# Optimization experiments

Measured on AMD Instinct MI355X. Metric: run time of the kernel, lower is better.

The kernel has to match this reference:

```python
import jax, jax.numpy as jnp
import numpy as np

E = 2          # e_layers
DM = 64        # d_model == emb_dim (hardcoded 64 in out_layer)
H = 8          # n_heads
DH = DM // H
DFF = 256      # d_ff
P = 16         # patch_size
STRIDE = P // 2
SL = 4096      # seq_len
NPATCH = (SL - P) // STRIDE + 1   # 511
PRED = 96
B, M = 8, 8
FACTOR = 5
EPS = 1e-5


def setup_inputs() -> dict:
    key = jax.random.key(0)
    ks = jax.random.split(key, 32)
    s = jnp.float32(0.02)
    f = lambda i, shape: jax.random.normal(ks[i], shape, jnp.float32)
    d = {
        "x_enc": f(0, (B, SL, M)),
        "x_mark_enc": f(1, (B, SL, 4)),
        "x_dec": f(2, (B, PRED, M)),
        "x_mark_dec": f(3, (B, PRED, 4)),
        # patch embedding  Linear(patch_size -> emb_dim)
        "in_W": f(4, (DM, P)) * s,
        "in_b": jnp.zeros((DM,), jnp.float32),
        # per-layer attention projections (stacked over e_layers)
        "Wq": f(5, (E, DM, DM)) * s, "bq": jnp.zeros((E, DM), jnp.float32),
        "Wk": f(6, (E, DM, DM)) * s, "bk": jnp.zeros((E, DM), jnp.float32),
        "Wv": f(7, (E, DM, DM)) * s, "bv": jnp.zeros((E, DM), jnp.float32),
        "Wo": f(8, (E, DM, DM)) * s, "bo": jnp.zeros((E, DM), jnp.float32),
        # FFN (Conv1d kernel=1 == Linear)
        "c1_W": f(9, (E, DFF, DM)) * s, "c1_b": jnp.zeros((E, DFF), jnp.float32),
        "c2_W": f(10, (E, DM, DFF)) * s, "c2_b": jnp.zeros((E, DM), jnp.float32),
        # layer norms
        "ln1_g": jnp.ones((E, DM), jnp.float32), "ln1_b": jnp.zeros((E, DM), jnp.float32),
        "ln2_g": jnp.ones((E, DM), jnp.float32), "ln2_b": jnp.zeros((E, DM), jnp.float32),
        "lnf_g": jnp.ones((DM,), jnp.float32), "lnf_b": jnp.zeros((DM,), jnp.float32),
        # decode head  Linear(64*num_patches -> pred_len)
        "out_W": f(11, (PRED, DM * NPATCH)) * s,
        "out_b": jnp.zeros((PRED,), jnp.float32),
    }
    return d


def _ln(x, g, b):
    mu = x.mean(-1, keepdims=True)
    var = ((x - mu) ** 2).mean(-1, keepdims=True)
    return (x - mu) * jax.lax.rsqrt(var + EPS) * g + b


def _prob_attn(q, k, v, key):
    # q,k,v: [Bn, H, L, Dh]  (ProbSparse attention, mask_flag=False)
    Bn, h, Lq, Dh = q.shape
    Lk = k.shape[2]
    U_part = min(int(FACTOR * np.ceil(np.log(Lk))), Lk)   # sampled keys per query
    u = min(int(FACTOR * np.ceil(np.log(Lq))), Lq)        # top-u active queries
    idx = jax.random.randint(key, (Lq, U_part), 0, Lk)
    k_sample = k[:, :, idx, :]                             # [Bn,H,Lq,U,Dh]
    qk_sample = jnp.einsum('bhld,bhlud->bhlu', q, k_sample)
    # sparsity measure: max - sum/L_K (as in torch code)
    sparsity = qk_sample.max(-1) - qk_sample.sum(-1) / jnp.float32(Lk)
    _, top_idx = jax.lax.top_k(sparsity, u)                # [Bn,H,u]
    q_red = jnp.take_along_axis(q, top_idx[..., None], axis=2)  # [Bn,H,u,Dh]
    scale = jax.lax.rsqrt(jnp.float32(Dh))
    scores = jnp.einsum('bhud,bhkd->bhuk', q_red, k) * scale    # [Bn,H,u,Lk]
    attn = jax.nn.softmax(scores, axis=-1)
    # lazy context: mean of V for inactive queries, attn@V for active ones
    ctx = jnp.broadcast_to(v.mean(axis=2, keepdims=True), q.shape)
    upd = jnp.einsum('bhuk,bhkd->bhud', attn, v)
    bi = jnp.arange(Bn)[:, None, None]
    hi = jnp.arange(h)[None, :, None]
    ctx = ctx.at[bi, hi, top_idx].set(upd)
    return ctx.transpose(0, 2, 1, 3)  # [Bn,L,H,Dh]


def reference(x_enc, x_mark_enc, x_dec, x_mark_dec, in_W, in_b, Wq, bq, Wk, bk,
              Wv, bv, Wo, bo, c1_W, c1_b, c2_W, c2_b, ln1_g, ln1_b, ln2_g, ln2_b,
              lnf_g, lnf_b, out_W, out_b):
    Bb, L, Mm = x_enc.shape
    x = x_enc.transpose(0, 2, 1)  # b l m -> b m l
    pidx = jnp.arange(NPATCH)[:, None] * STRIDE + jnp.arange(P)[None, :]
    patches = x[:, :, pidx]                         # [B,M,N,P] (unfold)
    z = patches.reshape(Bb * Mm, NPATCH, P) @ in_W.T + in_b  # [BM,N,DM]
    akey = jax.random.key(1)
    for e in range(E):
        q = (z @ Wq[e].T + bq[e]).reshape(Bb * Mm, NPATCH, H, DH).transpose(0, 2, 1, 3)
        k = (z @ Wk[e].T + bk[e]).reshape(Bb * Mm, NPATCH, H, DH).transpose(0, 2, 1, 3)
        v = (z @ Wv[e].T + bv[e]).reshape(Bb * Mm, NPATCH, H, DH).transpose(0, 2, 1, 3)
        ctx = _prob_attn(q, k, v, jax.random.fold_in(akey, e))
        new_x = ctx.reshape(Bb * Mm, NPATCH, DM) @ Wo[e].T + bo[e]
        x1 = _ln(z + new_x, ln1_g[e], ln1_b[e])
        y = jax.nn.gelu(x1 @ c1_W[e].T + c1_b[e], approximate=False)
        y = y @ c2_W[e].T + c2_b[e]
        z = _ln(x1 + y, ln2_g[e], ln2_b[e])
    z = _ln(z, lnf_g, lnf_b)
    out = z.reshape(Bb * Mm, -1) @ out_W.T + out_b   # [BM, pred_len]
    out = out.reshape(Bb, Mm, PRED).transpose(0, 2, 1)  # (b m) l -> b l m
    return out[:, -PRED:, :]
```

## Files before the change

### kernel.cpp

```cpp
#include <hip/hip_runtime.h>
#include <hip/hip_bf16.h>
#include <stdint.h>
#include <math.h>

typedef __hip_bfloat16 bf16;
typedef __attribute__((ext_vector_type(8))) short short8;
typedef __attribute__((ext_vector_type(4))) short short4v;
typedef __attribute__((ext_vector_type(4))) float fx4;

#define NP 511
#define UPART 35
#define NTOK 32704
#define NBITS 17885
#define LN_EPS 1e-5f

__host__ __device__ __forceinline__ void tf2x32(uint32_t k0, uint32_t k1,
                                                uint32_t x0, uint32_t x1,
                                                uint32_t* o0, uint32_t* o1) {
  uint32_t ks2 = k0 ^ k1 ^ 0x1BD11BDAu;
  x0 += k0; x1 += k1;
#define TFR(r) { x0 += x1; x1 = (x1 << (r)) | (x1 >> (32 - (r))); x1 ^= x0; }
  TFR(13) TFR(15) TFR(26) TFR(6)   x0 += k1;  x1 += ks2 + 1u;
  TFR(17) TFR(29) TFR(16) TFR(24)  x0 += ks2; x1 += k0 + 2u;
  TFR(13) TFR(15) TFR(26) TFR(6)   x0 += k0;  x1 += k1 + 3u;
  TFR(17) TFR(29) TFR(16) TFR(24)  x0 += k1;  x1 += ks2 + 4u;
  TFR(13) TFR(15) TFR(26) TFR(6)   x0 += ks2; x1 += k0 + 5u;
#undef TFR
  *o0 = x0; *o1 = x1;
}

__device__ __forceinline__ float ldin(const void* p, int i, int f32) {
  if (f32) return ((const float*)p)[i];
  return __bfloat162float(((const bf16*)p)[i]);
}
__device__ __forceinline__ unsigned short f2bf(float v) {
  uint32_t u = __builtin_bit_cast(uint32_t, v);
  u += 0x7fffu + ((u >> 16) & 1u);
  return (unsigned short)(u >> 16);
}
__device__ __forceinline__ float bfb2f(uint32_t h) {
  uint32_t u = h << 16;
  return __builtin_bit_cast(float, u);
}
__device__ __forceinline__ float lo16(uint32_t w) { return bfb2f(w & 0xFFFFu); }
__device__ __forceinline__ float hi16(uint32_t w) { return bfb2f(w >> 16); }
__device__ __forceinline__ uint32_t pack2(float a, float b) {
  return (uint32_t)f2bf(a) | ((uint32_t)f2bf(b) << 16);
}
__device__ __forceinline__ int lanes_below(unsigned long long m) {
  return __builtin_amdgcn_mbcnt_hi((uint32_t)(m >> 32),
         __builtin_amdgcn_mbcnt_lo((uint32_t)m, 0));
}

__global__ void zero_out_kernel(bf16* __restrict__ out, int n) {
  int i = blockIdx.x * 256 + threadIdx.x;
  if (i < n) out[i] = __float2bfloat16(0.f);
}

__global__ void gen_idx_kernel(int* __restrict__ idxT,
    uint32_t ka0, uint32_t ka1, uint32_t kb0, uint32_t kb1,
    const uint32_t* __restrict__ lnfg, int* __restrict__ flag) {
  if (blockIdx.x == 0 && threadIdx.x == 0)
    flag[0] = (lnfg[0] == 0x3F800000u) ? 1 : 0;
  int i = blockIdx.x * 256 + threadIdx.x;
  if (i >= 2 * NBITS) return;
  int e = i / NBITS;
  uint32_t j = (uint32_t)(i - e * NBITS);
  uint32_t k0 = e ? kb0 : ka0, k1 = e ? kb1 : ka1;
  uint32_t o0, o1;
  tf2x32(k0, k1, 0u, j, &o0, &o1);
  uint32_t bits = o1;
  uint32_t hi = bits >> 16, lo = bits & 0xFFFFu;
  uint32_t off = ((hi % 511u) * 32u + (lo % 511u)) % 511u;
  int l = (int)(j / UPART), u = (int)(j % UPART);
  idxT[e * NBITS + u * NP + l] = (int)off;
}

__global__ __launch_bounds__(256) void embed_kernel(
    const void* __restrict__ xe, const void* __restrict__ inW,
    const void* __restrict__ inb, float* __restrict__ z,
    const int* __restrict__ flg) {
  __shared__ float xs[136 * 8];
  int f = flg[0];
  int b = blockIdx.x >> 5, nt = blockIdx.x & 31;
  int n0 = nt * 16;
  for (int i = threadIdx.x; i < 1088; i += 256) {
    int row = i >> 3, m = i & 7;
    int g = n0 * 8 + row;
    xs[i] = (g < 4096) ? ldin(xe, (b * 4096 + g) * 8 + m, f) : 0.f;
  }
  int d = threadIdx.x & 63, mg = threadIdx.x >> 6;
  float wreg[16];
#pragma unroll
  for (int p = 0; p < 16; ++p) wreg[p] = ldin(inW, d * 16 + p, f);
  float bd = ldin(inb, d, f);
  __syncthreads();
  for (int nl = 0; nl < 16; ++nl) {
    int n = n0 + nl;
    if (n >= NP) break;
#pragma unroll
    for (int mm = 0; mm < 2; ++mm) {
      int m = mg * 2 + mm;
      float acc = bd;
#pragma unroll
      for (int p = 0; p < 16; ++p)
        acc = fmaf(xs[(nl * 8 + p) * 8 + m], wreg[p], acc);
      int t = (b * 8 + m) * NP + n;
      z[(size_t)t * 64 + d] = acc;
    }
  }
}

__global__ __launch_bounds__(256) void qkv_kernel(
    const float* __restrict__ z,
    const void* __restrict__ Wq, const void* __restrict__ bq,
    const void* __restrict__ Wk, const void* __restrict__ bk,
    const void* __restrict__ Wv, const void* __restrict__ bv,
    bf16* __restrict__ qb, bf16* __restrict__ kb, bf16* __restrict__ vb,
    const int* __restrict__ flg, int e) {
  __shared__ short xb[64 * 72];
  __shared__ short wL[192 * 72];
  __shared__ float bqs[192];
  int f = flg[0];
  int t0 = blockIdx.x * 64;
  int tid = threadIdx.x;
  {
    const float4* xg = (const float4*)(z + (size_t)t0 * 64);
#pragma unroll
    for (int r = 0; r < 4; ++r) {
      int i4 = r * 256 + tid;
      float4 v = xg[i4];
      int t = (i4 * 4) >> 6, d = (i4 * 4) & 63;
      short4v h;
      h.x = (short)f2bf(v.x); h.y = (short)f2bf(v.y);
      h.z = (short)f2bf(v.z); h.w = (short)f2bf(v.w);
      *(short4v*)&xb[t * 72 + d] = h;
    }
  }
  if (!f) {
    const uint4* Wg0 = (const uint4*)((const bf16*)Wq + e * 4096);
    const uint4* Wg1 = (const uint4*)((const bf16*)Wk + e * 4096);
    const uint4* Wg2 = (const uint4*)((const bf16*)Wv + e * 4096);
#pragma unroll
    for (int r = 0; r < 2; ++r) {
      int i = r * 256 + tid;
      int row = i >> 3, c8 = (i & 7) * 8;
      *(uint4*)&wL[row * 72 + c8] = Wg0[i];
      *(uint4*)&wL[(64 + row) * 72 + c8] = Wg1[i];
      *(uint4*)&wL[(128 + row) * 72 + c8] = Wg2[i];
    }
  } else {
#pragma unroll
    for (int r = 0; r < 16; ++r) {
      int i = r * 256 + tid;
      int row = i >> 6, c = i & 63;
      wL[row * 72 + c] = (short)f2bf(((const float*)Wq)[e * 4096 + i]);
      wL[(64 + row) * 72 + c] = (short)f2bf(((const float*)Wk)[e * 4096 + i]);
      wL[(128 + row) * 72 + c] = (short)f2bf(((const float*)Wv)[e * 4096 + i]);
    }
  }
  if (tid < 192) {
    int t3 = tid >> 6, j = tid & 63;
    bqs[tid] = (t3 == 0) ? ldin(bq, e * 64 + j, f)
             : (t3 == 1) ? ldin(bk, e * 64 + j, f)
                         : ldin(bv, e * 64 + j, f);
  }
  __syncthreads();
  int lane = tid & 63, w = tid >> 6;
  int m0 = w * 16, col = lane & 15, quad = lane >> 4;
  short8 a0 = *(const short8*)&xb[(m0 + col) * 72 + quad * 8];
  short8 a1 = *(const short8*)&xb[(m0 + col) * 72 + 32 + quad * 8];
#pragma unroll
  for (int nt = 0; nt < 12; ++nt) {
    fx4 acc = {0.f, 0.f, 0.f, 0.f};
    short8 b0 = *(const short8*)&wL[(nt * 16 + col) * 72 + quad * 8];
    short8 b1 = *(const short8*)&wL[(nt * 16 + col) * 72 + 32 + quad * 8];
    acc = __builtin_amdgcn_mfma_f32_16x16x32_bf16(a0, b0, acc, 0, 0, 0);
    acc = __builtin_amdgcn_mfma_f32_16x16x32_bf16(a1, b1, acc, 0, 0, 0);
    int c = nt * 16 + col;
    int t3 = c >> 6, hd = c & 63, h = hd >> 3, d2 = hd & 7;
    bf16* base = (t3 == 0) ? qb : (t3 == 1) ? kb : vb;
    float bia = bqs[c];
#pragma unroll
    for (int reg = 0; reg < 4; ++reg) {
      int tok = t0 + m0 + quad * 4 + reg;
      int bm = tok / NP, n = tok - bm * NP;
      base[((size_t)(bm * 8 + h) * NP + n) * 8 + d2] =
          __float2bfloat16(acc[reg] + bia);
    }
  }
}

__global__ __launch_bounds__(1024, 8) void attn_fused_kernel(
    const bf16* __restrict__ qg, const bf16* __restrict__ kg,
    const bf16* __restrict__ vg, const int* __restrict__ idxT,
    bf16* __restrict__ ctx) {
  __shared__ uint32_t kkp[NP * 5 + 5];
  __shared__ uint32_t kvp[NP * 5 + 5];
  __shared__ float spars[512];
  __shared__ float mxB_s[512], smB_s[512];
  __shared__ float redv[256];
  __shared__ int topi[UPART];
  __shared__ float vmean[8];
  __shared__ unsigned char selflag[NP + 1];
  int bh = blockIdx.x;
  int bm = bh >> 3, h = bh & 7;
  size_t hb = (size_t)bh * NP * 8;
  int tid = threadIdx.x;
  int lane = tid & 63, wv = tid >> 6;
  if (tid < 512) {
    if (tid < NP) {
      uint4 b = ((const uint4*)(kg + hb))[tid];
      uint32_t* dk = kkp + tid * 5;
      dk[0] = b.x; dk[1] = b.y; dk[2] = b.z; dk[3] = b.w;
    }
  } else {
    int n = tid - 512;
    if (n < NP) {
      uint4 c = ((const uint4*)(vg + hb))[n];
      uint32_t* dv = kvp + n * 5;
      dv[0] = c.x; dv[1] = c.y; dv[2] = c.z; dv[3] = c.w;
    }
  }
  __syncthreads();
  float mxA = -1e30f, smA = 0.f;
  if (tid < NP) {
    int l = tid;
    uint4 a = ((const uint4*)(qg + hb))[l];
    float ql[8];
    ql[0] = lo16(a.x); ql[1] = hi16(a.x);
    ql[2] = lo16(a.y); ql[3] = hi16(a.y);
    ql[4] = lo16(a.z); ql[5] = hi16(a.z);
    ql[6] = lo16(a.w); ql[7] = hi16(a.w);
#pragma unroll 6
    for (int u = 0; u < 18; ++u) {
      int j = idxT[u * NP + l];
      j = ((unsigned)j > 510u) ? 0 : j;
      const uint32_t* kr = kkp + j * 5;
      uint32_t w0 = kr[0], w1 = kr[1], w2 = kr[2], w3 = kr[3];
      float dt = 0.f;
      dt = fmaf(ql[0], lo16(w0), dt); dt = fmaf(ql[1], hi16(w0), dt);
      dt = fmaf(ql[2], lo16(w1), dt); dt = fmaf(ql[3], hi16(w1), dt);
      dt = fmaf(ql[4], lo16(w2), dt); dt = fmaf(ql[5], hi16(w2), dt);
      dt = fmaf(ql[6], lo16(w3), dt); dt = fmaf(ql[7], hi16(w3), dt);
      mxA = fmaxf(mxA, dt); smA += dt;
    }
  } else if (tid >= 512 && tid < 512 + NP) {
    int l = tid - 512;
    uint4 a = ((const uint4*)(qg + hb))[l];
    float ql[8];
    ql[0] = lo16(a.x); ql[1] = hi16(a.x);
    ql[2] = lo16(a.y); ql[3] = hi16(a.y);
    ql[4] = lo16(a.z); ql[5] = hi16(a.z);
    ql[6] = lo16(a.w); ql[7] = hi16(a.w);
    float mxB = -1e30f, smB = 0.f;
#pragma unroll 6
    for (int u = 18; u < 35; ++u) {
      int j = idxT[u * NP + l];
      j = ((unsigned)j > 510u) ? 0 : j;
      const uint32_t* kr = kkp + j * 5;
      uint32_t w0 = kr[0], w1 = kr[1], w2 = kr[2], w3 = kr[3];
      float dt = 0.f;
      dt = fmaf(ql[0], lo16(w0), dt); dt = fmaf(ql[1], hi16(w0), dt);
      dt = fmaf(ql[2], lo16(w1), dt); dt = fmaf(ql[3], hi16(w1), dt);
      dt = fmaf(ql[4], lo16(w2), dt); dt = fmaf(ql[5], hi16(w2), dt);
      dt = fmaf(ql[6], lo16(w3), dt); dt = fmaf(ql[7], hi16(w3), dt);
      mxB = fmaxf(mxB, dt); smB += dt;
    }
    mxB_s[l] = mxB; smB_s[l] = smB;
  }
  __syncthreads();
  if (tid < NP) {
    spars[tid] = fmaxf(mxA, mxB_s[tid]) - (smA + smB_s[tid]) * (1.0f / 511.0f);
  } else if (tid >= 512 && tid < 768) {
    int tt = tid - 512;
    int d = tt & 7, pt = tt >> 3;
    int c = d >> 1, odd = d & 1;
    float s = 0.f;
    for (int n = pt; n < NP; n += 32) {
      uint32_t w = kvp[n * 5 + c];
      s += odd ? hi16(w) : lo16(w);
    }
    redv[tt] = s;
  }
  __syncthreads();
  if (tid < 64) {
    uint32_t key[8];
#pragma unroll
    for (int jj = 0; jj < 8; ++jj) {
      int ll = lane + jj * 64;
      if (ll < NP) {
        uint32_t u = __builtin_bit_cast(uint32_t, spars[ll]);
        key[jj] = (u & 0x80000000u) ? ~u : (u | 0x80000000u);
      } else key[jj] = 0u;
    }
    uint32_t p = 0u;
    for (int b = 31; b >= 0; --b) {
      uint32_t t = p | (1u << b);
      int cnt = 0;
#pragma unroll
      for (int jj = 0; jj < 8; ++jj)
        cnt += __popcll(__ballot(key[jj] >= t));
      if (cnt >= UPART) p = t;
    }
    int c1 = 0;
#pragma unroll
    for (int jj = 0; jj < 8; ++jj)
      c1 += __popcll(__ballot(key[jj] > p));
    int need = UPART - c1;
    int base = 0, taken = 0;
#pragma unroll
    for (int jj = 0; jj < 8; ++jj) {
      int ll = lane + jj * 64;
      bool gt = key[jj] > p;
      bool eq = key[jj] == p;
      unsigned long long meq = __ballot(eq);
      int beq = lanes_below(meq);
      bool sel = gt || (eq && (taken + beq) < need);
      unsigned long long msel = __ballot(sel);
      int pos = base + lanes_below(msel);
      if (sel) topi[pos] = ll;
      if (ll < NP) selflag[ll] = sel ? 1 : 0;
      base += __popcll(msel);
      taken += __popcll(meq);
    }
  } else if (tid >= 64 && tid < 72) {
    int d = tid - 64;
    float s = 0.f;
#pragma unroll
    for (int pt = 0; pt < 32; ++pt) s += redv[pt * 8 + d];
    vmean[d] = s * (1.0f / 511.0f);
  }
  __syncthreads();
  size_t cb = (size_t)bm * (NP * 64) + h * 8;
  if (tid < NP && !selflag[tid]) {
    uint4 pv;
    pv.x = pack2(vmean[0], vmean[1]);
    pv.y = pack2(vmean[2], vmean[3]);
    pv.z = pack2(vmean[4], vmean[5]);
    pv.w = pack2(vmean[6], vmean[7]);
    *(uint4*)(ctx + cb + (size_t)tid * 64) = pv;
  }
  const float scale = 0.35355339059327373f;
  int l0 = topi[wv];
  int l1 = topi[wv + 16];
  bool has3 = (wv + 32) < UPART;
  int l2 = has3 ? topi[wv + 32] : l0;
  l0 = ((unsigned)l0 > 510u) ? 0 : l0;
  l1 = ((unsigned)l1 > 510u) ? 0 : l1;
  l2 = ((unsigned)l2 > 510u) ? 0 : l2;
  const uint4* q4p = (const uint4*)(qg + hb);
  uint4 qv0 = q4p[l0];
  uint4 qv1 = q4p[l1];
  uint4 qv2 = q4p[l2];

  auto process = [&](uint4 a, int lsel) {
    float qs[8];
    qs[0] = lo16(a.x); qs[1] = hi16(a.x);
    qs[2] = lo16(a.y); qs[3] = hi16(a.y);
    qs[4] = lo16(a.z); qs[5] = hi16(a.z);
    qs[6] = lo16(a.w); qs[7] = hi16(a.w);
    float sreg[8];
    float mx = -1e30f;
#pragma unroll
    for (int s = 0; s < 8; ++s) {
      int j = lane + s * 64;
      int jc = (j > 510) ? 0 : j;
      const uint32_t* kr = kkp + jc * 5;
      uint32_t w0 = kr[0], w1 = kr[1], w2 = kr[2], w3 = kr[3];
      float d0 = qs[0] * lo16(w0);
      d0 = fmaf(qs[1], hi16(w0), d0);
      d0 = fmaf(qs[2], lo16(w1), d0);
      d0 = fmaf(qs[3], hi16(w1), d0);
      float d1 = qs[4] * lo16(w2);
      d1 = fmaf(qs[5], hi16(w2), d1);
      d1 = fmaf(qs[6], lo16(w3), d1);
      d1 = fmaf(qs[7], hi16(w3), d1);
      float sc = (d0 + d1) * scale;
      sreg[s] = (j > 510) ? -1e30f : sc;
      mx = fmaxf(mx, sreg[s]);
    }
    for (int off = 32; off; off >>= 1) mx = fmaxf(mx, __shfl_xor(mx, off));
    float ssum = 0.f, acc[8];
#pragma unroll
    for (int d2 = 0; d2 < 8; ++d2) acc[d2] = 0.f;
#pragma unroll
    for (int s = 0; s < 8; ++s) {
      int j = lane + s * 64;
      int jc = (j > 510) ? 0 : j;
      float w = __expf(sreg[s] - mx);
      ssum += w;
      const uint32_t* vr = kvp + jc * 5;
      uint32_t x0 = vr[0], x1 = vr[1], x2 = vr[2], x3 = vr[3];
      acc[0] = fmaf(w, lo16(x0), acc[0]); acc[1] = fmaf(w, hi16(x0), acc[1]);
      acc[2] = fmaf(w, lo16(x1), acc[2]); acc[3] = fmaf(w, hi16(x1), acc[3]);
      acc[4] = fmaf(w, lo16(x2), acc[4]); acc[5] = fmaf(w, hi16(x2), acc[5]);
      acc[6] = fmaf(w, lo16(x3), acc[6]); acc[7] = fmaf(w, hi16(x3), acc[7]);
    }
    for (int off = 32; off; off >>= 1) {
      ssum += __shfl_xor(ssum, off);
#pragma unroll
      for (int d2 = 0; d2 < 8; ++d2) acc[d2] += __shfl_xor(acc[d2], off);
    }
    if (lane == 0) {
      float inv = 1.0f / ssum;
      uint4 pv;
      pv.x = pack2(acc[0] * inv, acc[1] * inv);
      pv.y = pack2(acc[2] * inv, acc[3] * inv);
      pv.z = pack2(acc[4] * inv, acc[5] * inv);
      pv.w = pack2(acc[6] * inv, acc[7] * inv);
      *(uint4*)(ctx + cb + (size_t)lsel * 64) = pv;
    }
  };
  process(qv0, l0);
  process(qv1, l1);
  if (has3) process(qv2, l2);
}

__global__ __launch_bounds__(256) void oproj_ln_kernel(
    const float* __restrict__ z, const bf16* __restrict__ ctx,
    const void* __restrict__ Wo, const void* __restrict__ bo,
    const void* __restrict__ g, const void* __restrict__ bb,
    float* __restrict__ x1, const int* __restrict__ flg, int e) {
  __shared__ short cbL[64 * 72];
  __shared__ short woL[64 * 72];
  __shared__ float zf[64 * 64];
  __shared__ float bos[64], gs[64], bbs[64];
  int f = flg[0];
  int t0 = blockIdx.x * 64;
  int tid = threadIdx.x;
  {
    const uint4* cg = (const uint4*)(ctx + (size_t)t0 * 64);
#pragma unroll
    for (int r = 0; r < 2; ++r) {
      int i = r * 256 + tid;
      uint4 v = cg[i];
      int row = i >> 3, c8 = (i & 7) * 8;
      *(uint4*)&cbL[row * 72 + c8] = v;
    }
    const float4* zg = (const float4*)(z + (size_t)t0 * 64);
#pragma unroll
    for (int r = 0; r < 4; ++r) {
      int i4 = r * 256 + tid;
      float4 v = zg[i4];
      int t = (i4 * 4) >> 6, d = (i4 * 4) & 63;
      *(float4*)&zf[t * 64 + d] = v;
    }
  }
  if (!f) {
    const uint4* Wg = (const uint4*)((const bf16*)Wo + e * 4096);
#pragma unroll
    for (int r = 0; r < 2; ++r) {
      int i = r * 256 + tid;
      int row = i >> 3, c8 = (i & 7) * 8;
      *(uint4*)&woL[row * 72 + c8] = Wg[i];
    }
  } else {
#pragma unroll
    for (int r = 0; r < 16; ++r) {
      int i = r * 256 + tid;
      int row = i >> 6, c = i & 63;
      woL[row * 72 + c] = (short)f2bf(((const float*)Wo)[e * 4096 + i]);
    }
  }
  if (tid < 64) {
    bos[tid] = ldin(bo, e * 64 + tid, f);
    gs[tid] = ldin(g, e * 64 + tid, f);
    bbs[tid] = ldin(bb, e * 64 + tid, f);
  }
  __syncthreads();
  int lane = tid & 63, w = tid >> 6;
  int m0 = w * 16, col = lane & 15, quad = lane >> 4;
  short8 a0 = *(const short8*)&cbL[(m0 + col) * 72 + quad * 8];
  short8 a1 = *(const short8*)&cbL[(m0 + col) * 72 + 32 + quad * 8];
  fx4 vacc[4];
#pragma unroll
  for (int nt = 0; nt < 4; ++nt) {
    fx4 acc = {0.f, 0.f, 0.f, 0.f};
    short8 b0 = *(const short8*)&woL[(nt * 16 + col) * 72 + quad * 8];
    short8 b1 = *(const short8*)&woL[(nt * 16 + col) * 72 + 32 + quad * 8];
    acc = __builtin_amdgcn_mfma_f32_16x16x32_bf16(a0, b0, acc, 0, 0, 0);
    acc = __builtin_amdgcn_mfma_f32_16x16x32_bf16(a1, b1, acc, 0, 0, 0);
    vacc[nt] = acc;
  }
  float vals[4][4];
  float ps[4], sq[4];
#pragma unroll
  for (int reg = 0; reg < 4; ++reg) { ps[reg] = 0.f; sq[reg] = 0.f; }
#pragma unroll
  for (int nt = 0; nt < 4; ++nt) {
    int d = nt * 16 + col;
#pragma unroll
    for (int reg = 0; reg < 4; ++reg) {
      int tl = m0 + quad * 4 + reg;
      float v = vacc[nt][reg] + bos[d] + zf[tl * 64 + d];
      vals[nt][reg] = v;
      ps[reg] += v; sq[reg] += v * v;
    }
  }
#pragma unroll
  for (int off = 1; off < 16; off <<= 1) {
#pragma unroll
    for (int reg = 0; reg < 4; ++reg) {
      ps[reg] += __shfl_xor(ps[reg], off);
      sq[reg] += __shfl_xor(sq[reg], off);
    }
  }
#pragma unroll
  for (int reg = 0; reg < 4; ++reg) {
    float mu = ps[reg] * (1.0f / 64.0f);
    float var = sq[reg] * (1.0f / 64.0f) - mu * mu;
    float rs = rsqrtf(fmaxf(var, 0.f) + LN_EPS);
    int tl = m0 + quad * 4 + reg;
#pragma unroll
    for (int nt = 0; nt < 4; ++nt) {
      int d = nt * 16 + col;
      x1[(size_t)(t0 + tl) * 64 + d] = (vals[nt][reg] - mu) * rs * gs[d] + bbs[d];
    }
  }
}

__global__ __launch_bounds__(256) void ffn_kernel(
    const float* __restrict__ x1,
    const void* __restrict__ W1, const void* __restrict__ b1,
    const void* __restrict__ W2, const void* __restrict__ b2,
    const void* __restrict__ g, const void* __restrict__ bb,
    float* __restrict__ zo, bf16* __restrict__ zfT,
    const void* __restrict__ lfg, const void* __restrict__ lfb,
    const int* __restrict__ flg, int e, int last) {
  __shared__ __align__(16) char smem[72960];
  short* wA  = (short*)smem;
  short* rB  = (short*)(smem + 36864);
  float* b1s = (float*)(smem + 70656);
  float* b2s = b1s + 256;
  float* gs  = b2s + 64;
  float* bbs = gs + 64;
  float* g2s = bbs + 64;
  float* bb2s = g2s + 64;
  int f = flg[0];
  int t0 = blockIdx.x * 64;
  int tid = threadIdx.x;
  {
    const float4* xg = (const float4*)(x1 + (size_t)t0 * 64);
#pragma unroll
    for (int r = 0; r < 4; ++r) {
      int i4 = r * 256 + tid;
      float4 v = xg[i4];
      int t = (i4 * 4) >> 6, d = (i4 * 4) & 63;
      short4v h;
      h.x = (short)f2bf(v.x); h.y = (short)f2bf(v.y);
      h.z = (short)f2bf(v.z); h.w = (short)f2bf(v.w);
      *(short4v*)&rB[t * 72 + d] = h;
    }
  }
  if (!f) {
    const uint4* W1g = (const uint4*)((const bf16*)W1 + e * 16384);
#pragma unroll
    for (int r = 0; r < 8; ++r) {
      int i = r * 256 + tid;
      uint4 v = W1g[i];
      int j = i >> 3, k = (i & 7) * 8;
      *(uint4*)&wA[j * 72 + k] = v;
    }
  } else {
    for (int r = 0; r < 64; ++r) {
      int i = r * 256 + tid;
      int j = i >> 6, k = i & 63;
      wA[j * 72 + k] = (short)f2bf(((const float*)W1)[e * 16384 + i]);
    }
  }
  b1s[tid] = ldin(b1, e * 256 + tid, f);
  if (tid < 64) {
    b2s[tid] = ldin(b2, e * 64 + tid, f);
    gs[tid] = ldin(g, e * 64 + tid, f);
    bbs[tid] = ldin(bb, e * 64 + tid, f);
    g2s[tid] = ldin(lfg, tid, f);
    bb2s[tid] = ldin(lfb, tid, f);
  }
  __syncthreads();

  int lane = tid & 63, w = tid >> 6;
  int m0 = w * 16;
  int col = lane & 15, quad = lane >> 4;
  short8 a0 = *(const short8*)&rB[(m0 + col) * 72 + quad * 8];
  short8 a1 = *(const short8*)&rB[(m0 + col) * 72 + 32 + quad * 8];
  __syncthreads();
#pragma unroll 4
  for (int nt = 0; nt < 16; ++nt) {
    fx4 acc = {0.f, 0.f, 0.f, 0.f};
    short8 bf0 = *(const short8*)&wA[(nt * 16 + col) * 72 + quad * 8];
    short8 bf1 = *(const short8*)&wA[(nt * 16 + col) * 72 + 32 + quad * 8];
    acc = __builtin_amdgcn_mfma_f32_16x16x32_bf16(a0, bf0, acc, 0, 0, 0);
    acc = __builtin_amdgcn_mfma_f32_16x16x32_bf16(a1, bf1, acc, 0, 0, 0);
    int j = nt * 16 + col;
    float bj = b1s[j];
#pragma unroll
    for (int reg = 0; reg < 4; ++reg) {
      float a = acc[reg] + bj;
      float ge = 0.5f * a * (1.0f + erff(a * 0.70710678118654752f));
      rB[(m0 + quad * 4 + reg) * 264 + j] = (short)f2bf(ge);
    }
  }
  __syncthreads();
  if (!f) {
    const uint4* W2g = (const uint4*)((const bf16*)W2 + e * 16384);
#pragma unroll
    for (int r = 0; r < 8; ++r) {
      int i = r * 256 + tid;
      uint4 v2 = W2g[i];
      int dd = i >> 5, c = (i & 31) * 8;
      *(uint4*)&wA[dd * 264 + c] = v2;
    }
  } else {
    for (int r = 0; r < 64; ++r) {
      int i = r * 256 + tid;
      int dd = i >> 8, c = i & 255;
      wA[dd * 264 + c] = (short)f2bf(((const float*)W2)[e * 16384 + i]);
    }
  }
  __syncthreads();
  short8 af[8];
#pragma unroll
  for (int kt = 0; kt < 8; ++kt)
    af[kt] = *(const short8*)&rB[(m0 + col) * 264 + kt * 32 + quad * 8];
  fx4 vacc[4];
#pragma unroll
  for (int nt = 0; nt < 4; ++nt) {
    fx4 acc = {0.f, 0.f, 0.f, 0.f};
#pragma unroll
    for (int kt = 0; kt < 8; ++kt) {
      short8 bfr = *(const short8*)&wA[(nt * 16 + col) * 264 + kt * 32 + quad * 8];
      acc = __builtin_amdgcn_mfma_f32_16x16x32_bf16(af[kt], bfr, acc, 0, 0, 0);
    }
    vacc[nt] = acc;
  }
  float vals[4][4];
  float ps[4], sq[4];
#pragma unroll
  for (int reg = 0; reg < 4; ++reg) { ps[reg] = 0.f; sq[reg] = 0.f; }
#pragma unroll
  for (int nt = 0; nt < 4; ++nt) {
    int d = nt * 16 + col;
#pragma unroll
    for (int reg = 0; reg < 4; ++reg) {
      int tl = m0 + quad * 4 + reg;
      float v = vacc[nt][reg] + b2s[d] + x1[(size_t)(t0 + tl) * 64 + d];
      vals[nt][reg] = v;
      ps[reg] += v; sq[reg] += v * v;
    }
  }
#pragma unroll
  for (int off = 1; off < 16; off <<= 1) {
#pragma unroll
    for (int reg = 0; reg < 4; ++reg) {
      ps[reg] += __shfl_xor(ps[reg], off);
      sq[reg] += __shfl_xor(sq[reg], off);
    }
  }
  if (!last) {
#pragma unroll
    for (int reg = 0; reg < 4; ++reg) {
      float mu = ps[reg] * (1.0f / 64.0f);
      float var = sq[reg] * (1.0f / 64.0f) - mu * mu;
      float rs = rsqrtf(fmaxf(var, 0.f) + LN_EPS);
      int tl = m0 + quad * 4 + reg;
#pragma unroll
      for (int nt = 0; nt < 4; ++nt) {
        int d = nt * 16 + col;
        zo[(size_t)(t0 + tl) * 64 + d] = (vals[nt][reg] - mu) * rs * gs[d] + bbs[d];
      }
    }
  } else {
    float ps2[4], sq2[4];
#pragma unroll
    for (int reg = 0; reg < 4; ++reg) { ps2[reg] = 0.f; sq2[reg] = 0.f; }
    float v2s[4][4];
#pragma unroll
    for (int reg = 0; reg < 4; ++reg) {
      float mu = ps[reg] * (1.0f / 64.0f);
      float var = sq[reg] * (1.0f / 64.0f) - mu * mu;
      float rs = rsqrtf(fmaxf(var, 0.f) + LN_EPS);
#pragma unroll
      for (int nt = 0; nt < 4; ++nt) {
        int d = nt * 16 + col;
        float v2 = (vals[nt][reg] - mu) * rs * gs[d] + bbs[d];
        v2s[nt][reg] = v2;
        ps2[reg] += v2; sq2[reg] += v2 * v2;
      }
    }
#pragma unroll
    for (int off = 1; off < 16; off <<= 1) {
#pragma unroll
      for (int reg = 0; reg < 4; ++reg) {
        ps2[reg] += __shfl_xor(ps2[reg], off);
        sq2[reg] += __shfl_xor(sq2[reg], off);
      }
    }
#pragma unroll
    for (int reg = 0; reg < 4; ++reg) {
      float mu = ps2[reg] * (1.0f / 64.0f);
      float var = sq2[reg] * (1.0f / 64.0f) - mu * mu;
      float rs = rsqrtf(fmaxf(var, 0.f) + LN_EPS);
      int tok = t0 + m0 + quad * 4 + reg;
      int bm = tok / NP, n = tok - bm * NP;
#pragma unroll
      for (int nt = 0; nt < 4; ++nt) {
        int d = nt * 16 + col;
        zfT[(size_t)n * 4096 + bm * 64 + d] =
            __float2bfloat16((v2s[nt][reg] - mu) * rs * g2s[d] + bb2s[d]);
      }
    }
  }
}

__global__ __launch_bounds__(256) void head1_kernel(
    const bf16* __restrict__ zfT, const void* __restrict__ W,
    float* __restrict__ partial, const int* __restrict__ flg) {
  __shared__ short aL[64 * 72];
  __shared__ short bL[96 * 72];
  int f = flg[0];
  int n = blockIdx.x;
  int tid = threadIdx.x;
  {
    const uint4* Ag = (const uint4*)(zfT + (size_t)n * 4096);
#pragma unroll
    for (int r = 0; r < 2; ++r) {
      int i = r * 256 + tid;
      uint4 v = Ag[i];
      int row = i >> 3, c = (i & 7) * 8;
      *(uint4*)&aL[row * 72 + c] = v;
    }
  }
  if (!f) {
    const uint4* Wg = (const uint4*)W;
#pragma unroll
    for (int r = 0; r < 3; ++r) {
      int i = r * 256 + tid;
      int p = i >> 3, c8 = i & 7;
      uint4 v = Wg[(size_t)p * 4088 + n * 8 + c8];
      *(uint4*)&bL[p * 72 + c8 * 8] = v;
    }
  } else {
    for (int r = 0; r < 24; ++r) {
      int i = r * 256 + tid;
      int p = i >> 6, c = i & 63;
      bL[p * 72 + c] = (short)f2bf(((const float*)W)[(size_t)p * 32704 + n * 64 + c]);
    }
  }
  __syncthreads();
  int lane = tid & 63, w = tid >> 6;
  int m0 = w * 16, col = lane & 15, quad = lane >> 4;
  short8 a0 = *(const short8*)&aL[(m0 + col) * 72 + quad * 8];
  short8 a1 = *(const short8*)&aL[(m0 + col) * 72 + 32 + quad * 8];
  float* pb = partial + (size_t)n * 6144;
#pragma unroll
  for (int nt = 0; nt < 6; ++nt) {
    fx4 acc = {0.f, 0.f, 0.f, 0.f};
    short8 b0 = *(const short8*)&bL[(nt * 16 + col) * 72 + quad * 8];
    short8 b1 = *(const short8*)&bL[(nt * 16 + col) * 72 + 32 + quad * 8];
    acc = __builtin_amdgcn_mfma_f32_16x16x32_bf16(a0, b0, acc, 0, 0, 0);
    acc = __builtin_amdgcn_mfma_f32_16x16x32_bf16(a1, b1, acc, 0, 0, 0);
#pragma unroll
    for (int reg = 0; reg < 4; ++reg)
      pb[(m0 + quad * 4 + reg) * 96 + nt * 16 + col] = acc[reg];
  }
}

__global__ __launch_bounds__(256) void head2_kernel(
    const float* __restrict__ partial, const void* __restrict__ bias,
    void* __restrict__ out, const int* __restrict__ flg) {
  __shared__ float red[4][64];
  int f = flg[0];
  int lane = threadIdx.x & 63, w = threadIdx.x >> 6;
  int j = blockIdx.x * 64 + lane;
  float acc = 0.f;
  for (int n = w; n < NP; n += 4)
    acc += partial[(size_t)n * 6144 + j];
  red[w][lane] = acc;
  __syncthreads();
  if (w == 0) {
    float s = red[0][lane] + red[1][lane] + red[2][lane] + red[3][lane];
    int bm = j / 96, p = j - bm * 96;
    float val = s + ldin(bias, p, f);
    int b = bm >> 3, m = bm & 7;
    int o = (b * 96 + p) * 8 + m;
    if (f) ((float*)out)[o] = val;
    else   ((bf16*)out)[o] = __float2bfloat16(val);
  }
}

extern "C" void kernel_launch(void* const* d_in, const int* in_sizes, int n_in,
                              void* d_out, int out_size, void* d_ws, size_t ws_size,
                              hipStream_t stream) {
  const void* xe  = d_in[0];
  const void* inW = d_in[4];
  const void* inb = d_in[5];
  const void* Wq  = d_in[6];
  const void* bq  = d_in[7];
  const void* Wk  = d_in[8];
  const void* bk  = d_in[9];
  const void* Wv  = d_in[10];
  const void* bv  = d_in[11];
  const void* Wo  = d_in[12];
  const void* bo  = d_in[13];
  const void* c1W = d_in[14];
  const void* c1b = d_in[15];
  const void* c2W = d_in[16];
  const void* c2b = d_in[17];
  const void* l1g = d_in[18];
  const void* l1b = d_in[19];
  const void* l2g = d_in[20];
  const void* l2b = d_in[21];
  const void* lfg = d_in[22];
  const void* lfb = d_in[23];
  const void* oW  = d_in[24];
  const void* obv = d_in[25];

  const size_t NF = (size_t)NTOK * 64;
  const size_t REQ = (3 * NF + 2 * NBITS + 32) * sizeof(float);
  if (ws_size < REQ) {
    zero_out_kernel<<<(out_size + 255) / 256, 256, 0, stream>>>((bf16*)d_out, out_size);
    return;
  }

  float* z   = (float*)d_ws;
  bf16* ctxb = (bf16*)(z + NF);
  bf16* qb   = (bf16*)(z + NF + NF / 2);
  bf16* kb   = (bf16*)(z + 2 * NF);
  bf16* vb   = (bf16*)(z + 2 * NF + NF / 2);
  float* x1  = z + 2 * NF;
  int* idxb  = (int*)(z + 3 * NF);
  int* flg   = idxb + 2 * NBITS;
  bf16* zfT  = ctxb;
  float* partial = z;

  uint32_t ke[2][2];
  for (int e = 0; e < 2; ++e)
    tf2x32(0u, 1u, 0u, (uint32_t)e, &ke[e][0], &ke[e][1]);
  gen_idx_kernel<<<(2 * NBITS + 255) / 256, 256, 0, stream>>>(idxb,
      ke[0][0], ke[0][1], ke[1][0], ke[1][1], (const uint32_t*)lfg, flg);

  embed_kernel<<<256, 256, 0, stream>>>(xe, inW, inb, z, flg);
  for (int e = 0; e < 2; ++e) {
    qkv_kernel<<<NTOK / 64, 256, 0, stream>>>(z, Wq, bq, Wk, bk, Wv, bv,
        qb, kb, vb, flg, e);
    attn_fused_kernel<<<512, 1024, 0, stream>>>(qb, kb, vb, idxb + e * NBITS,
        ctxb);
    oproj_ln_kernel<<<NTOK / 64, 256, 0, stream>>>(z, ctxb, Wo, bo, l1g, l1b,
        x1, flg, e);
    ffn_kernel<<<NTOK / 64, 256, 0, stream>>>(x1, c1W, c1b, c2W, c2b,
        l2g, l2b, z, zfT, lfg, lfb, flg, e, e == 1);
  }
  head1_kernel<<<NP, 256, 0, stream>>>(zfT, oW, partial, flg);
  head2_kernel<<<96, 256, 0, stream>>>(partial, obv, d_out, flg);
}
```

Measured before the change: 311.8 us.

## Fuse output projection and first layernorm into the FFN kernel

Merges the attention output projection plus residual layernorm kernel into the FFN kernel, keeping the normalized activations in registers and shared memory instead of writing them to a global fp32 buffer. This removes one kernel launch per layer and the global write and reread of the intermediate activations. Shared memory is reused across phases with an extra barrier, and the kernel needs a slightly larger LDS allocation.

```diff
diff --git a/kernel.cpp b/kernel.cpp
--- a/kernel.cpp
+++ b/kernel.cpp
@@ -417,156 +417,66 @@
   if (has3) process(qv2, l2);
 }
 
-__global__ __launch_bounds__(256) void oproj_ln_kernel(
+__global__ __launch_bounds__(256) void oproj_ffn_kernel(
     const float* __restrict__ z, const bf16* __restrict__ ctx,
     const void* __restrict__ Wo, const void* __restrict__ bo,
-    const void* __restrict__ g, const void* __restrict__ bb,
-    float* __restrict__ x1, const int* __restrict__ flg, int e) {
-  __shared__ short cbL[64 * 72];
-  __shared__ short woL[64 * 72];
-  __shared__ float zf[64 * 64];
-  __shared__ float bos[64], gs[64], bbs[64];
-  int f = flg[0];
-  int t0 = blockIdx.x * 64;
-  int tid = threadIdx.x;
-  {
-    const uint4* cg = (const uint4*)(ctx + (size_t)t0 * 64);
-#pragma unroll
-    for (int r = 0; r < 2; ++r) {
-      int i = r * 256 + tid;
-      uint4 v = cg[i];
-      int row = i >> 3, c8 = (i & 7) * 8;
-      *(uint4*)&cbL[row * 72 + c8] = v;
-    }
-    const float4* zg = (const float4*)(z + (size_t)t0 * 64);
-#pragma unroll
-    for (int r = 0; r < 4; ++r) {
-      int i4 = r * 256 + tid;
-      float4 v = zg[i4];
-      int t = (i4 * 4) >> 6, d = (i4 * 4) & 63;
-      *(float4*)&zf[t * 64 + d] = v;
-    }
-  }
-  if (!f) {
-    const uint4* Wg = (const uint4*)((const bf16*)Wo + e * 4096);
-#pragma unroll
-    for (int r = 0; r < 2; ++r) {
-      int i = r * 256 + tid;
-      int row = i >> 3, c8 = (i & 7) * 8;
-      *(uint4*)&woL[row * 72 + c8] = Wg[i];
-    }
-  } else {
-#pragma unroll
-    for (int r = 0; r < 16; ++r) {
-      int i = r * 256 + tid;
-      int row = i >> 6, c = i & 63;
-      woL[row * 72 + c] = (short)f2bf(((const float*)Wo)[e * 4096 + i]);
-    }
-  }
-  if (tid < 64) {
-    bos[tid] = ldin(bo, e * 64 + tid, f);
-    gs[tid] = ldin(g, e * 64 + tid, f);
-    bbs[tid] = ldin(bb, e * 64 + tid, f);
-  }
-  __syncthreads();
-  int lane = tid & 63, w = tid >> 6;
-  int m0 = w * 16, col = lane & 15, quad = lane >> 4;
-  short8 a0 = *(const short8*)&cbL[(m0 + col) * 72 + quad * 8];
-  short8 a1 = *(const short8*)&cbL[(m0 + col) * 72 + 32 + quad * 8];
-  fx4 vacc[4];
-#pragma unroll
-  for (int nt = 0; nt < 4; ++nt) {
-    fx4 acc = {0.f, 0.f, 0.f, 0.f};
-    short8 b0 = *(const short8*)&woL[(nt * 16 + col) * 72 + quad * 8];
-    short8 b1 = *(const short8*)&woL[(nt * 16 + col) * 72 + 32 + quad * 8];
-    acc = __builtin_amdgcn_mfma_f32_16x16x32_bf16(a0, b0, acc, 0, 0, 0);
-    acc = __builtin_amdgcn_mfma_f32_16x16x32_bf16(a1, b1, acc, 0, 0, 0);
-    vacc[nt] = acc;
-  }
-  float vals[4][4];
-  float ps[4], sq[4];
-#pragma unroll
-  for (int reg = 0; reg < 4; ++reg) { ps[reg] = 0.f; sq[reg] = 0.f; }
-#pragma unroll
-  for (int nt = 0; nt < 4; ++nt) {
-    int d = nt * 16 + col;
-#pragma unroll
-    for (int reg = 0; reg < 4; ++reg) {
-      int tl = m0 + quad * 4 + reg;
-      float v = vacc[nt][reg] + bos[d] + zf[tl * 64 + d];
-      vals[nt][reg] = v;
-      ps[reg] += v; sq[reg] += v * v;
-    }
-  }
-#pragma unroll
-  for (int off = 1; off < 16; off <<= 1) {
-#pragma unroll
-    for (int reg = 0; reg < 4; ++reg) {
-      ps[reg] += __shfl_xor(ps[reg], off);
-      sq[reg] += __shfl_xor(sq[reg], off);
-    }
-  }
-#pragma unroll
-  for (int reg = 0; reg < 4; ++reg) {
-    float mu = ps[reg] * (1.0f / 64.0f);
-    float var = sq[reg] * (1.0f / 64.0f) - mu * mu;
-    float rs = rsqrtf(fmaxf(var, 0.f) + LN_EPS);
-    int tl = m0 + quad * 4 + reg;
-#pragma unroll
-    for (int nt = 0; nt < 4; ++nt) {
-      int d = nt * 16 + col;
-      x1[(size_t)(t0 + tl) * 64 + d] = (vals[nt][reg] - mu) * rs * gs[d] + bbs[d];
-    }
-  }
-}
-
-__global__ __launch_bounds__(256) void ffn_kernel(
-    const float* __restrict__ x1,
+    const void* __restrict__ l1g, const void* __restrict__ l1b,
     const void* __restrict__ W1, const void* __restrict__ b1,
     const void* __restrict__ W2, const void* __restrict__ b2,
     const void* __restrict__ g, const void* __restrict__ bb,
     float* __restrict__ zo, bf16* __restrict__ zfT,
     const void* __restrict__ lfg, const void* __restrict__ lfb,
     const int* __restrict__ flg, int e, int last) {
-  __shared__ __align__(16) char smem[72960];
+  __shared__ __align__(16) char smem[73728];
+  short* cbL = (short*)smem;
+  short* woL = (short*)(smem + 9216);
+  float* zf  = (float*)(smem + 18432);
   short* wA  = (short*)smem;
   short* rB  = (short*)(smem + 36864);
   float* b1s = (float*)(smem + 70656);
-  float* b2s = b1s + 256;
-  float* gs  = b2s + 64;
-  float* bbs = gs + 64;
-  float* g2s = bbs + 64;
+  float* b2s  = b1s + 256;
+  float* gs   = b2s + 64;
+  float* bbs  = gs + 64;
+  float* g2s  = bbs + 64;
   float* bb2s = g2s + 64;
+  float* bos  = bb2s + 64;
+  float* g1s  = bos + 64;
+  float* bb1s = g1s + 64;
   int f = flg[0];
   int t0 = blockIdx.x * 64;
   int tid = threadIdx.x;
   {
-    const float4* xg = (const float4*)(x1 + (size_t)t0 * 64);
+    const uint4* cg = (const uint4*)(ctx + (size_t)t0 * 64);
+#pragma unroll
+    for (int r = 0; r < 2; ++r) {
+      int i = r * 256 + tid;
+      uint4 v = cg[i];
+      int row = i >> 3, c8 = (i & 7) * 8;
+      *(uint4*)&cbL[row * 72 + c8] = v;
+    }
+    const float4* zg = (const float4*)(z + (size_t)t0 * 64);
 #pragma unroll
     for (int r = 0; r < 4; ++r) {
       int i4 = r * 256 + tid;
-      float4 v = xg[i4];
+      float4 v = zg[i4];
       int t = (i4 * 4) >> 6, d = (i4 * 4) & 63;
-      short4v h;
-      h.x = (short)f2bf(v.x); h.y = (short)f2bf(v.y);
-      h.z = (short)f2bf(v.z); h.w = (short)f2bf(v.w);
-      *(short4v*)&rB[t * 72 + d] = h;
+      *(float4*)&zf[t * 64 + d] = v;
     }
   }
   if (!f) {
-    const uint4* W1g = (const uint4*)((const bf16*)W1 + e * 16384);
-#pragma unroll
-    for (int r = 0; r < 8; ++r) {
-      int i = r * 256 + tid;
-      uint4 v = W1g[i];
-      int j = i >> 3, k = (i & 7) * 8;
-      *(uint4*)&wA[j * 72 + k] = v;
+    const uint4* Wg = (const uint4*)((const bf16*)Wo + e * 4096);
+#pragma unroll
+    for (int r = 0; r < 2; ++r) {
+      int i = r * 256 + tid;
+      int row = i >> 3, c8 = (i & 7) * 8;
+      *(uint4*)&woL[row * 72 + c8] = Wg[i];
     }
   } else {
-    for (int r = 0; r < 64; ++r) {
-      int i = r * 256 + tid;
-      int j = i >> 6, k = i & 63;
-      wA[j * 72 + k] = (short)f2bf(((const float*)W1)[e * 16384 + i]);
+#pragma unroll
+    for (int r = 0; r < 16; ++r) {
+      int i = r * 256 + tid;
+      int row = i >> 6, c = i & 63;
+      woL[row * 72 + c] = (short)f2bf(((const float*)Wo)[e * 4096 + i]);
     }
   }
   b1s[tid] = ldin(b1, e * 256 + tid, f);
@@ -576,12 +486,87 @@
     bbs[tid] = ldin(bb, e * 64 + tid, f);
     g2s[tid] = ldin(lfg, tid, f);
     bb2s[tid] = ldin(lfb, tid, f);
-  }
-  __syncthreads();
-
+    bos[tid] = ldin(bo, e * 64 + tid, f);
+    g1s[tid] = ldin(l1g, e * 64 + tid, f);
+    bb1s[tid] = ldin(l1b, e * 64 + tid, f);
+  }
+  __syncthreads();
   int lane = tid & 63, w = tid >> 6;
-  int m0 = w * 16;
-  int col = lane & 15, quad = lane >> 4;
+  int m0 = w * 16, col = lane & 15, quad = lane >> 4;
+  float x1v[4][4];
+  {
+    short8 a0 = *(const short8*)&cbL[(m0 + col) * 72 + quad * 8];
+    short8 a1 = *(const short8*)&cbL[(m0 + col) * 72 + 32 + quad * 8];
+    fx4 vacc[4];
+#pragma unroll
+    for (int nt = 0; nt < 4; ++nt) {
+      fx4 acc = {0.f, 0.f, 0.f, 0.f};
+      short8 b0 = *(const short8*)&woL[(nt * 16 + col) * 72 + quad * 8];
+      short8 b1f = *(const short8*)&woL[(nt * 16 + col) * 72 + 32 + quad * 8];
+      acc = __builtin_amdgcn_mfma_f32_16x16x32_bf16(a0, b0, acc, 0, 0, 0);
+      acc = __builtin_amdgcn_mfma_f32_16x16x32_bf16(a1, b1f, acc, 0, 0, 0);
+      vacc[nt] = acc;
+    }
+    float vals[4][4];
+    float ps[4], sq[4];
+#pragma unroll
+    for (int reg = 0; reg < 4; ++reg) { ps[reg] = 0.f; sq[reg] = 0.f; }
+#pragma unroll
+    for (int nt = 0; nt < 4; ++nt) {
+      int d = nt * 16 + col;
+#pragma unroll
+      for (int reg = 0; reg < 4; ++reg) {
+        int tl = m0 + quad * 4 + reg;
+        float v = vacc[nt][reg] + bos[d] + zf[tl * 64 + d];
+        vals[nt][reg] = v;
+        ps[reg] += v; sq[reg] += v * v;
+      }
+    }
+#pragma unroll
+    for (int off = 1; off < 16; off <<= 1) {
+#pragma unroll
+      for (int reg = 0; reg < 4; ++reg) {
+        ps[reg] += __shfl_xor(ps[reg], off);
+        sq[reg] += __shfl_xor(sq[reg], off);
+      }
+    }
+#pragma unroll
+    for (int reg = 0; reg < 4; ++reg) {
+      float mu = ps[reg] * (1.0f / 64.0f);
+      float var = sq[reg] * (1.0f / 64.0f) - mu * mu;
+      float rs = rsqrtf(fmaxf(var, 0.f) + LN_EPS);
+#pragma unroll
+      for (int nt = 0; nt < 4; ++nt) {
+        int d = nt * 16 + col;
+        x1v[nt][reg] = (vals[nt][reg] - mu) * rs * g1s[d] + bb1s[d];
+      }
+    }
+#pragma unroll
+    for (int nt = 0; nt < 4; ++nt) {
+#pragma unroll
+      for (int reg = 0; reg < 4; ++reg) {
+        int tl = m0 + quad * 4 + reg;
+        rB[tl * 72 + nt * 16 + col] = (short)f2bf(x1v[nt][reg]);
+      }
+    }
+  }
+  __syncthreads();
+  if (!f) {
+    const uint4* W1g = (const uint4*)((const bf16*)W1 + e * 16384);
+#pragma unroll
+    for (int r = 0; r < 8; ++r) {
+      int i = r * 256 + tid;
+      uint4 v = W1g[i];
+      int j = i >> 3, k = (i & 7) * 8;
+      *(uint4*)&wA[j * 72 + k] = v;
+    }
+  } else {
+    for (int r = 0; r < 64; ++r) {
+      int i = r * 256 + tid;
+      int j = i >> 6, k = i & 63;
+      wA[j * 72 + k] = (short)f2bf(((const float*)W1)[e * 16384 + i]);
+    }
+  }
   short8 a0 = *(const short8*)&rB[(m0 + col) * 72 + quad * 8];
   short8 a1 = *(const short8*)&rB[(m0 + col) * 72 + 32 + quad * 8];
   __syncthreads();
@@ -643,8 +628,7 @@
     int d = nt * 16 + col;
 #pragma unroll
     for (int reg = 0; reg < 4; ++reg) {
-      int tl = m0 + quad * 4 + reg;
-      float v = vacc[nt][reg] + b2s[d] + x1[(size_t)(t0 + tl) * 64 + d];
+      float v = vacc[nt][reg] + b2s[d] + x1v[nt][reg];
       vals[nt][reg] = v;
       ps[reg] += v; sq[reg] += v * v;
     }
@@ -828,7 +812,6 @@
   bf16* qb   = (bf16*)(z + NF + NF / 2);
   bf16* kb   = (bf16*)(z + 2 * NF);
   bf16* vb   = (bf16*)(z + 2 * NF + NF / 2);
-  float* x1  = z + 2 * NF;
   int* idxb  = (int*)(z + 3 * NF);
   int* flg   = idxb + 2 * NBITS;
   bf16* zfT  = ctxb;
@@ -846,10 +829,8 @@
         qb, kb, vb, flg, e);
     attn_fused_kernel<<<512, 1024, 0, stream>>>(qb, kb, vb, idxb + e * NBITS,
         ctxb);
-    oproj_ln_kernel<<<NTOK / 64, 256, 0, stream>>>(z, ctxb, Wo, bo, l1g, l1b,
-        x1, flg, e);
-    ffn_kernel<<<NTOK / 64, 256, 0, stream>>>(x1, c1W, c1b, c2W, c2b,
-        l2g, l2b, z, zfT, lfg, lfb, flg, e, e == 1);
+    oproj_ffn_kernel<<<NTOK / 64, 256, 0, stream>>>(z, ctxb, Wo, bo, l1g, l1b,
+        c1W, c1b, c2W, c2b, l2g, l2b, z, zfT, lfg, lfb, flg, e, e == 1);
   }
   head1_kernel<<<NP, 256, 0, stream>>>(zfT, oW, partial, flg);
   head2_kernel<<<96, 256, 0, stream>>>(partial, obv, d_out, flg);
```

Result: faster. 298.6 us (-4.3%).
